# Optimization experiments

Measured on AMD Instinct MI355X. Metric: run time of the kernel, lower is better.

Reference implementation:

```python
import jax, jax.numpy as jnp
import numpy as np

CELL = 14
NC = 80
BPC = 3
IMG = 448.0
CS = IMG / CELL  # cell pixel size
CLASS_SCALE = 1.0
OBJECT_SCALE = 1.0
NOOBJECT_SCALE = 0.5
COORD_SCALE = 5.0
EPS = 1e-9

# base_boxes[y, x, b, :] = (x*CS, y*CS, 0, 0)
_gy, _gx = jnp.meshgrid(jnp.arange(CELL, dtype=jnp.float32), jnp.arange(CELL, dtype=jnp.float32), indexing='ij')
BASE = jnp.broadcast_to(jnp.stack([_gx * CS, _gy * CS, jnp.zeros_like(_gx), jnp.zeros_like(_gx)], axis=-1)[:, :, None, :], (CELL, CELL, BPC, 4))
MULT = jnp.array([CS, CS, IMG, IMG], dtype=jnp.float32)


def _ciou(boxes1, box2):
    # boxes1: [S,S,BPC,4] (cx,cy,w,h); box2: [4]
    b1_cx, b1_cy, b1_w, b1_h = boxes1[..., 0], boxes1[..., 1], boxes1[..., 2], boxes1[..., 3]
    b2_cx, b2_cy, b2_w, b2_h = box2[0], box2[1], box2[2], box2[3]
    b1_x1, b1_y1, b1_x2, b1_y2 = b1_cx - b1_w / 2, b1_cy - b1_h / 2, b1_cx + b1_w / 2, b1_cy + b1_h / 2
    b2_x1, b2_y1, b2_x2, b2_y2 = b2_cx - b2_w / 2, b2_cy - b2_h / 2, b2_cx + b2_w / 2, b2_cy + b2_h / 2
    inter = jnp.clip(jnp.minimum(b1_x2, b2_x2) - jnp.maximum(b1_x1, b2_x1), 0) * \
            jnp.clip(jnp.minimum(b1_y2, b2_y2) - jnp.maximum(b1_y1, b2_y1), 0)
    union = b1_w * b1_h + b2_w * b2_h - inter
    iou = inter / (union + EPS)
    center_distance = (b1_cx - b2_cx) ** 2 + (b1_cy - b2_cy) ** 2
    # faithful to original (uses center/size components for the enclosing box)
    enclose_left = jnp.minimum(boxes1[..., 0], box2[0])
    enclose_right = jnp.maximum(boxes1[..., 2], box2[2])
    enclose_top = jnp.minimum(boxes1[..., 1], box2[1])
    enclose_bottom = jnp.maximum(boxes1[..., 3], box2[3])
    enclose_diag = (enclose_right - enclose_left) ** 2 + (enclose_bottom - enclose_top) ** 2
    v = (4.0 / jnp.pi ** 2) * (jnp.arctan(b2_w / (b2_h + EPS)) - jnp.arctan(b1_w / (b1_h + EPS))) ** 2
    alpha = jax.lax.stop_gradient(v / (1 - iou + v + EPS))
    return iou - center_distance / (enclose_diag + EPS) - alpha * v  # [S,S,BPC]


def _l2(t):
    return 0.5 * jnp.sum(t * t)


def _per_object_loss(predict, label):
    # predict: [S,S,NC+5*BPC], label: [5]
    gy = jnp.arange(CELL, dtype=jnp.float32)[:, None]
    gx = jnp.arange(CELL, dtype=jnp.float32)[None, :]
    x, y, w, h = label[0], label[1], label[2], label[3]
    min_x = jnp.floor((x - w / 2) / CS)
    max_x = jnp.minimum(jnp.ceil((x + w / 2) / CS), CELL)
    min_y = jnp.floor((y - h / 2) / CS)
    max_y = jnp.minimum(jnp.ceil((y + h / 2) / CS), CELL)
    object_mask = ((gx >= min_x) & (gx < max_x) & (gy >= min_y) & (gy < max_y)).astype(jnp.float32)
    cx, cy = jnp.floor(x / CS), jnp.floor(y / CS)
    center_mask = ((gx == cx) & (gy == cy)).astype(jnp.float32)

    pboxes = predict[:, :, NC + BPC:].reshape(CELL, CELL, BPC, 4) * MULT + BASE
    iou = _ciou(pboxes, label[:4])                     # [S,S,BPC]
    C = iou * center_mask[..., None]
    I = (iou >= jnp.max(iou, axis=-1, keepdims=True)).astype(jnp.float32) * center_mask[..., None]
    no_I = 1.0 - I
    p_C = predict[:, :, NC:NC + BPC]

    sqrt_w, sqrt_h = jnp.sqrt(jnp.abs(w)), jnp.sqrt(jnp.abs(h))
    p_x, p_y = pboxes[..., 0], pboxes[..., 1]
    p_sqrt_w = jnp.sqrt(jnp.clip(pboxes[..., 2], 0.0, IMG))
    p_sqrt_h = jnp.sqrt(jnp.clip(pboxes[..., 3], 0.0, IMG))

    P = jax.nn.one_hot(label[4].astype(jnp.int32), NC, dtype=jnp.float32)
    p_P = predict[:, :, :NC]

    class_loss = _l2(object_mask[..., None] * (p_P - P)) * CLASS_SCALE
    object_loss = _l2(I * (p_C - C)) * OBJECT_SCALE
    noobject_loss = _l2(no_I * p_C) * NOOBJECT_SCALE
    coord_loss = (_l2(I * (p_x - x) / CS) + _l2(I * (p_y - y) / CS)
                  + _l2(I * (p_sqrt_w - sqrt_w)) / IMG + _l2(I * (p_sqrt_h - sqrt_h)) / IMG) * COORD_SCALE
    return class_loss + object_loss + noobject_loss + coord_loss


def setup_inputs() -> dict:
    key = jax.random.key(0)
    k1, k2, k3, k4, k5 = jax.random.split(key, 5)
    B, M = 1024, 30
    predicts = jax.random.normal(k1, (B, CELL, CELL, NC + 5 * BPC), dtype=jnp.float32) * 0.1
    xy = jax.random.uniform(k2, (B, M, 2), minval=60.0, maxval=IMG - 60.0)
    wh = jax.random.uniform(k3, (B, M, 2), minval=10.0, maxval=100.0)
    cls = jax.random.randint(k4, (B, M, 1), 0, NC).astype(jnp.float32)
    labels = jnp.concatenate([xy, wh, cls], axis=-1)
    objects_num = jax.random.randint(k5, (B,), 1, M + 1).astype(jnp.int32)
    return {"predicts": predicts, "labels": labels, "objects_num": objects_num}


def reference(predicts, labels, objects_num):
    B, M = labels.shape[0], labels.shape[1]
    per_batch = jax.vmap(lambda p, ls: jax.vmap(lambda l: _per_object_loss(p, l))(ls))
    losses = per_batch(predicts, labels)  # [B, M]
    mask = (jnp.arange(M)[None, :] < objects_num[:, None]).astype(jnp.float32)
    return jnp.sum(losses * mask) / B
```

## Files before the change

kernel.cpp:

```cpp
#include <hip/hip_runtime.h>
#include <math.h>

#define CELLN 14
#define NCELLS 196
#define NCLS 80
#define NCH 95
#define NDW (NCELLS * NCH)
#define NF4 (NDW / 4)
#define NW32 (NCELLS * 20)

__global__ __launch_bounds__(256) void yolo_loss_kernel(
    const float* __restrict__ predicts,
    const float* __restrict__ labels,
    const int* __restrict__ objects_num,
    float* __restrict__ out,
    int M, float invB)
{
    __shared__ unsigned s_W32[NW32];
    __shared__ float    s_cnt[NCELLS];
    __shared__ float    s_red[4];

    const int img  = blockIdx.x;
    const int tid  = threadIdx.x;
    const int lane = tid & 63;
    const int wid  = tid >> 6;
    const float inv32 = 1.0f / 32.0f;

    const float*  gpred = predicts + (size_t)img * NDW;
    const float4* gp4   = (const float4*)gpred;
    const int n = objects_num[img];

    for (int i = tid; i < NW32; i += 256) s_W32[i] = 0u;
    for (int i = tid; i < NCELLS; i += 256) s_cnt[i] = 0.0f;
    __syncthreads();

    float acc = 0.0f;
    for (int g = (tid >> 3); g < n; g += 32) {
        const int r = tid & 7;
        const float* lab = labels + ((size_t)img * M + g) * 5;
        const float x = lab[0], y = lab[1], w = lab[2], h = lab[3];
        const int cls = (int)lab[4];

        int min_x = max(0, (int)floorf((x - w * 0.5f) * inv32));
        int max_x = min(CELLN, (int)ceilf((x + w * 0.5f) * inv32));
        int min_y = max(0, (int)floorf((y - h * 0.5f) * inv32));
        int max_y = min(CELLN, (int)ceilf((y + h * 0.5f) * inv32));
        int nx = max_x - min_x;
        int ncell = nx * (max_y - min_y);

        if (r == 0) acc += 0.5f * (float)ncell;
        const unsigned winc = 1u << (8 * (cls & 3));
        const int      woff = cls >> 2;
        for (int p = r; p < ncell; p += 8) {
            int cell = (min_y + p / nx) * CELLN + (min_x + p % nx);
            atomicAdd(&s_cnt[cell], 1.0f);
            atomicAdd(&s_W32[cell * 20 + woff], winc);
        }
    }
    __syncthreads();

    float pc2 = 0.0f;
    #pragma unroll
    for (int i = 0; i < 19; ++i) {
        int f = tid + (i << 8);
        if (f < NF4) {
            float4 v4 = gp4[f];
            unsigned idx  = (unsigned)f << 2;
            unsigned cell = idx / 95u;
            unsigned ch   = idx - cell * 95u;
            float vv[4] = {v4.x, v4.y, v4.z, v4.w};
            #pragma unroll
            for (int k = 0; k < 4; ++k) {
                float v = vv[k];
                if (ch < (unsigned)NCLS) {
                    unsigned wword = s_W32[cell * 20 + (ch >> 2)];
                    float wgt = (float)((wword >> (8 * (ch & 3))) & 255u);
                    acc += 0.5f * s_cnt[cell] * v * v - wgt * v;
                } else if (ch < 83u) {
                    pc2 += v * v;
                }
                ++ch;
                if (ch == 95u) { ch = 0u; ++cell; }
            }
        }
    }
    acc += 0.25f * (float)n * pc2;

    for (int o = tid; o < n; o += 256) {
        const float* lab = labels + ((size_t)img * M + o) * 5;
        const float x = lab[0], y = lab[1], w = lab[2], h = lab[3];

        int cx = (int)floorf(x * inv32);
        int cy = (int)floorf(y * inv32);
        const float* cp = gpred + (cy * CELLN + cx) * NCH;
        float bx = (float)cx * 32.0f;
        float by = (float)cy * 32.0f;

        float pC[3], ciou[3], pxv[3], pyv[3], pwv[3], phv[3];
        #pragma unroll
        for (int b = 0; b < 3; ++b) {
            pC[b] = cp[NCLS + b];
            float px = cp[83 + 4*b] * 32.0f + bx;
            float py = cp[84 + 4*b] * 32.0f + by;
            float pw = cp[85 + 4*b] * 448.0f;
            float ph = cp[86 + 4*b] * 448.0f;
            pxv[b] = px; pyv[b] = py; pwv[b] = pw; phv[b] = ph;
            float iw = fminf(px + pw*0.5f, x + w*0.5f) - fmaxf(px - pw*0.5f, x - w*0.5f);
            float ih = fminf(py + ph*0.5f, y + h*0.5f) - fmaxf(py - ph*0.5f, y - h*0.5f);
            iw = fmaxf(iw, 0.0f); ih = fmaxf(ih, 0.0f);
            float inter = iw * ih;
            float uni = pw*ph + w*h - inter;
            float iou = inter / (uni + 1e-9f);
            float cd = (px - x)*(px - x) + (py - y)*(py - y);
            float el = fminf(px, x), er = fmaxf(pw, w);
            float et = fminf(py, y), eb = fmaxf(ph, h);
            float ed = (er - el)*(er - el) + (eb - et)*(eb - et);
            float da = atanf(w / (h + 1e-9f)) - atanf(pw / (ph + 1e-9f));
            float v = 0.40528473456935108577f * da * da;
            float alpha = v / (1.0f - iou + v + 1e-9f);
            ciou[b] = iou - cd / (ed + 1e-9f) - alpha * v;
        }
        float mx = fmaxf(ciou[0], fmaxf(ciou[1], ciou[2]));
        float sqw = sqrtf(fabsf(w)), sqh = sqrtf(fabsf(h));
        float sel_obj = 0.0f, sel_pc2 = 0.0f, coord = 0.0f;
        #pragma unroll
        for (int b = 0; b < 3; ++b) {
            if (ciou[b] >= mx) {
                float d = pC[b] - ciou[b];
                sel_obj += d * d;
                sel_pc2 += pC[b] * pC[b];
                float dx = (pxv[b] - x) * inv32;
                float dy = (pyv[b] - y) * inv32;
                float psw = sqrtf(fminf(fmaxf(pwv[b], 0.0f), 448.0f));
                float psh = sqrtf(fminf(fmaxf(phv[b], 0.0f), 448.0f));
                float dw = psw - sqw, dh = psh - sqh;
                coord += dx*dx + dy*dy + (dw*dw + dh*dh) * (1.0f/448.0f);
            }
        }
        acc += 0.5f * sel_obj - 0.25f * sel_pc2 + 2.5f * coord;
    }

    #pragma unroll
    for (int off = 32; off; off >>= 1) acc += __shfl_down(acc, off);
    if (lane == 0) s_red[wid] = acc;
    __syncthreads();
    if (tid == 0) {
        atomicAdd(out, (s_red[0] + s_red[1] + s_red[2] + s_red[3]) * invB);
    }
}

extern "C" void kernel_launch(void* const* d_in, const int* in_sizes, int n_in,
                              void* d_out, int out_size, void* d_ws, size_t ws_size,
                              hipStream_t stream) {
    const float* predicts = (const float*)d_in[0];
    const float* labels   = (const float*)d_in[1];
    const int*   objn     = (const int*)d_in[2];
    float* out = (float*)d_out;

    const int B = in_sizes[2];
    const int M = in_sizes[1] / (B * 5);

    yolo_loss_kernel<<<dim3(B), dim3(256), 0, stream>>>(
        predicts, labels, objn, out, M, 1.0f / (float)B);
}
```

Measured before the change: 124.9 us.

## Replace per-cell class weight histogram with direct gather of target class logits

Removes the packed per-cell class-count shared histogram and its second atomic per covered cell. The linear class term is now computed by each object's threads gathering the target class prediction directly from global memory for each covered cell. The streaming pass uses a single per-cell coefficient (half count, or a constant for confidence channels) with branchless FMAs split across two accumulators. It also sets a minimum of 4 blocks per CU in the launch bounds. Shared memory shrinks and the inner loop loses its bit unpacking, at the cost of scattered uncoalesced global reads, which should mostly hit cache.

```diff
diff --git a/kernel.cpp b/kernel.cpp
--- a/kernel.cpp
+++ b/kernel.cpp
@@ -7,18 +7,16 @@
 #define NCH 95
 #define NDW (NCELLS * NCH)
 #define NF4 (NDW / 4)
-#define NW32 (NCELLS * 20)
 
-__global__ __launch_bounds__(256) void yolo_loss_kernel(
+__global__ __launch_bounds__(256, 4) void yolo_loss_kernel(
     const float* __restrict__ predicts,
     const float* __restrict__ labels,
     const int* __restrict__ objects_num,
     float* __restrict__ out,
     int M, float invB)
 {
-    __shared__ unsigned s_W32[NW32];
-    __shared__ float    s_cnt[NCELLS];
-    __shared__ float    s_red[4];
+    __shared__ float s_half[NCELLS + 1];
+    __shared__ float s_red[4];
 
     const int img  = blockIdx.x;
     const int tid  = threadIdx.x;
@@ -30,11 +28,55 @@
     const float4* gp4   = (const float4*)gpred;
     const int n = objects_num[img];
 
-    for (int i = tid; i < NW32; i += 256) s_W32[i] = 0u;
-    for (int i = tid; i < NCELLS; i += 256) s_cnt[i] = 0.0f;
+    for (int i = tid; i < NCELLS + 1; i += 256) s_half[i] = 0.0f;
     __syncthreads();
 
     float acc = 0.0f;
+    for (int g = (tid >> 3); g < n; g += 32) {
+        const int r = tid & 7;
+        const float* lab = labels + ((size_t)img * M + g) * 5;
+        const float x = lab[0], y = lab[1], w = lab[2], h = lab[3];
+
+        int min_x = max(0, (int)floorf((x - w * 0.5f) * inv32));
+        int max_x = min(CELLN, (int)ceilf((x + w * 0.5f) * inv32));
+        int min_y = max(0, (int)floorf((y - h * 0.5f) * inv32));
+        int max_y = min(CELLN, (int)ceilf((y + h * 0.5f) * inv32));
+        int nx = max_x - min_x;
+        int ncell = nx * (max_y - min_y);
+
+        if (r == 0) acc += 0.5f * (float)ncell;
+        for (int p = r; p < ncell; p += 8) {
+            int cell = (min_y + p / nx) * CELLN + (min_x + p % nx);
+            atomicAdd(&s_half[cell], 0.5f);
+        }
+    }
+    __syncthreads();
+
+    const float qn = 0.25f * (float)n;
+    float acc2 = 0.0f;
+    #pragma unroll
+    for (int i = 0; i < 19; ++i) {
+        int f = tid + (i << 8);
+        if (f < NF4) {
+            float4 v4 = gp4[f];
+            unsigned idx  = (unsigned)f << 2;
+            unsigned cell = idx / 95u;
+            unsigned ch   = idx - cell * 95u;
+            float vv[4] = {v4.x, v4.y, v4.z, v4.w};
+            #pragma unroll
+            for (int k = 0; k < 4; ++k) {
+                float cnt = s_half[cell];
+                float c = (ch < 80u) ? cnt : ((ch < 83u) ? qn : 0.0f);
+                float v = vv[k];
+                if (k & 1) acc2 = fmaf(c * v, v, acc2);
+                else       acc  = fmaf(c * v, v, acc);
+                ++ch;
+                if (ch == 95u) { ch = 0u; ++cell; }
+            }
+        }
+    }
+    acc += acc2;
+
     for (int g = (tid >> 3); g < n; g += 32) {
         const int r = tid & 7;
         const float* lab = labels + ((size_t)img * M + g) * 5;
@@ -48,43 +90,13 @@
         int nx = max_x - min_x;
         int ncell = nx * (max_y - min_y);
 
-        if (r == 0) acc += 0.5f * (float)ncell;
-        const unsigned winc = 1u << (8 * (cls & 3));
-        const int      woff = cls >> 2;
+        float csum = 0.0f;
         for (int p = r; p < ncell; p += 8) {
             int cell = (min_y + p / nx) * CELLN + (min_x + p % nx);
-            atomicAdd(&s_cnt[cell], 1.0f);
-            atomicAdd(&s_W32[cell * 20 + woff], winc);
+            csum += gpred[cell * NCH + cls];
         }
+        acc -= csum;
     }
-    __syncthreads();
-
-    float pc2 = 0.0f;
-    #pragma unroll
-    for (int i = 0; i < 19; ++i) {
-        int f = tid + (i << 8);
-        if (f < NF4) {
-            float4 v4 = gp4[f];
-            unsigned idx  = (unsigned)f << 2;
-            unsigned cell = idx / 95u;
-            unsigned ch   = idx - cell * 95u;
-            float vv[4] = {v4.x, v4.y, v4.z, v4.w};
-            #pragma unroll
-            for (int k = 0; k < 4; ++k) {
-                float v = vv[k];
-                if (ch < (unsigned)NCLS) {
-                    unsigned wword = s_W32[cell * 20 + (ch >> 2)];
-                    float wgt = (float)((wword >> (8 * (ch & 3))) & 255u);
-                    acc += 0.5f * s_cnt[cell] * v * v - wgt * v;
-                } else if (ch < 83u) {
-                    pc2 += v * v;
-                }
-                ++ch;
-                if (ch == 95u) { ch = 0u; ++cell; }
-            }
-        }
-    }
-    acc += 0.25f * (float)n * pc2;
 
     for (int o = tid; o < n; o += 256) {
         const float* lab = labels + ((size_t)img * M + o) * 5;
```

Result: faster. 119.1 us (-4.7%).
